# Kernel optimization log

Measured on AMD Instinct MI355X. Metric: run time of the kernel, lower is better.

The kernel has to match this reference:

```python
import jax, jax.numpy as jnp
import numpy as np

K = 3  # involution kernel size


def dwconv3x3(x, w, b):
    # x: [B,C,H,W], w: [C,1,3,3] (depthwise, groups=C), b: [C]
    y = jax.lax.conv_general_dilated(
        x, w, window_strides=(1, 1), padding='SAME',
        dimension_numbers=('NCHW', 'OIHW', 'NCHW'),
        feature_group_count=x.shape[1])
    return y + b[None, :, None, None]


def conv1x1(x, w, b):
    # x: [B,C,H,W], w: [O,C], b: [O]
    return jnp.einsum('oc,bchw->bohw', w, x) + b[None, :, None, None]


def extract_patches(x):
    # x: [B,C,H,W] -> [B,C,K*K,H,W], zero-padded 'same' 3x3 neighborhoods
    B, C, H, W = x.shape
    p = (K - 1) // 2
    xp = jnp.pad(x, ((0, 0), (0, 0), (p, p), (p, p)))
    return jnp.stack([xp[:, :, i:i + H, j:j + W]
                      for i in range(K) for j in range(K)], axis=2)


def involution(x, w_red, b_red, w_span, b_span):
    # dynamic per-pixel kernels: [B, K*K, H, W]
    kern = conv1x1(jax.nn.relu(conv1x1(x, w_red, b_red)), w_span, b_span)
    patches = extract_patches(x)                 # [B,C,KK,H,W]
    return jnp.einsum('bkhw,bckhw->bchw', kern, patches)


def setup_inputs() -> dict:
    key = jax.random.key(0)
    ks = jax.random.split(key, 10)
    dim, red = 256, 64  # reduction ratio 4
    B, H, W = 8, 64, 64
    s = 0.05
    return {
        'x': jax.random.normal(ks[0], (B, dim, H, W), jnp.float32),
        'w_in': jax.random.normal(ks[1], (dim, 1, 3, 3), jnp.float32) * s,
        'b_in': jax.random.normal(ks[2], (dim,), jnp.float32) * s,
        'w_red': jax.random.normal(ks[3], (red, dim), jnp.float32) * s,
        'b_red': jax.random.normal(ks[4], (red,), jnp.float32) * s,
        'w_span': jax.random.normal(ks[5], (K * K, red), jnp.float32) * s,
        'b_span': jax.random.normal(ks[6], (K * K,), jnp.float32) * s,
        'w_out': jax.random.normal(ks[7], (dim, 1, 3, 3), jnp.float32) * s,
        'b_out': jax.random.normal(ks[8], (dim,), jnp.float32) * s,
    }


def reference(x, w_in, b_in, w_red, b_red, w_span, b_span, w_out, b_out):
    x = dwconv3x3(x, w_in, b_in)
    x = involution(x, w_red, b_red, w_span, b_span)
    x = dwconv3x3(x, w_out, b_out)
    return x
```

## Files before the change

kernel.cpp:

```cpp
#include <hip/hip_runtime.h>

#define BB 8
#define CC 256
#define HH 64
#define WW 64
#define RED 64
#define HW 4096
#define XS 68
#define LS 68

__global__ __launch_bounds__(256) void transpose_wred(const float* __restrict__ w_red,
                                                      float* __restrict__ wt) {
    int idx = blockIdx.x * 256 + threadIdx.x;
    int o = idx >> 8, c = idx & 255;
    wt[c * RED + o] = w_red[idx];
}

__global__ __launch_bounds__(512, 4) void dw_kern(const float* __restrict__ x,
                                                  const float* __restrict__ w_in,
                                                  const float* __restrict__ b_in,
                                                  const float* __restrict__ wt,
                                                  const float* __restrict__ b_red,
                                                  const float* __restrict__ w_span,
                                                  const float* __restrict__ b_span,
                                                  float* __restrict__ kern) {
    __shared__ float smem[4352 + 2 * 4096];
    float* xs   = smem;
    float* wbuf = smem + 4352;
    float* part = smem;

    const int t  = threadIdx.x;
    const int bx = blockIdx.x;
    const int h  = ((bx & 7) << 3) | (bx >> 3);
    const int b  = blockIdx.y;
    const int px = t & 63;
    const int og = t >> 6;
    const int o0 = __builtin_amdgcn_readfirstlane(og << 3);
    const int q  = t & 15;
    const int w0 = q << 2;
    const int cr = t >> 4;

    float4 pv[2][3]; float plf[2][3], prt[2][3];
    float4 wv0, wv1;

    auto loadX = [&](int c0) {
        #pragma unroll
        for (int s = 0; s < 2; s++) {
            const int cc = c0 + s * 32 + cr;
            const float* xp = x + ((size_t)(b * CC + cc)) * HW;
            #pragma unroll
            for (int ky = 0; ky < 3; ky++) {
                int hh = h + ky - 1;
                if (hh < 0 || hh >= HH) {
                    pv[s][ky] = make_float4(0.f, 0.f, 0.f, 0.f);
                    plf[s][ky] = 0.f; prt[s][ky] = 0.f;
                    continue;
                }
                const float* row = xp + hh * WW + w0;
                pv[s][ky]  = *(const float4*)row;
                plf[s][ky] = (w0 > 0)      ? row[-1] : 0.f;
                prt[s][ky] = (w0 + 4 < WW) ? row[4]  : 0.f;
            }
        }
    };
    auto loadW = [&](int c0) {
        const float* wp = wt + c0 * RED + t * 8;
        wv0 = *(const float4*)wp;
        wv1 = *(const float4*)(wp + 4);
    };
    auto computeX = [&](int c0) {
        #pragma unroll
        for (int s = 0; s < 2; s++) {
            const int cl = s * 32 + cr;
            const int cc = c0 + cl;
            const float* wp = w_in + cc * 9;
            const float bb = b_in[cc];
            float4 a4 = make_float4(bb, bb, bb, bb);
            #pragma unroll
            for (int ky = 0; ky < 3; ky++) {
                float4 v = pv[s][ky];
                float lf = plf[s][ky], rt = prt[s][ky];
                float k0 = wp[ky * 3 + 0], k1 = wp[ky * 3 + 1], k2 = wp[ky * 3 + 2];
                a4.x = fmaf(k0, lf,  a4.x); a4.y = fmaf(k0, v.x, a4.y);
                a4.z = fmaf(k0, v.y, a4.z); a4.w = fmaf(k0, v.z, a4.w);
                a4.x = fmaf(k1, v.x, a4.x); a4.y = fmaf(k1, v.y, a4.y);
                a4.z = fmaf(k1, v.z, a4.z); a4.w = fmaf(k1, v.w, a4.w);
                a4.x = fmaf(k2, v.y, a4.x); a4.y = fmaf(k2, v.z, a4.y);
                a4.z = fmaf(k2, v.w, a4.z); a4.w = fmaf(k2, rt,  a4.w);
            }
            *(float4*)&xs[cl * XS + w0] = a4;
        }
    };
    auto storeW = [&](int buf) {
        float* wb = wbuf + buf * 4096 + t * 8;
        *(float4*)wb = wv0;
        *(float4*)(wb + 4) = wv1;
    };

    float acc[8];
    #pragma unroll
    for (int i = 0; i < 8; i++) acc[i] = 0.f;

    loadX(0); loadW(0);
    computeX(0); storeW(0);
    __syncthreads();

    for (int k = 0; k < 4; k++) {
        if (k < 3) { loadX((k + 1) << 6); loadW((k + 1) << 6); }
        const float* wb = wbuf + (k & 1) * 4096 + o0;
        #pragma unroll 8
        for (int c = 0; c < 64; c++) {
            float xv = xs[c * XS + px];
            float4 wa = *(const float4*)(wb + c * 64);
            float4 wc = *(const float4*)(wb + c * 64 + 4);
            acc[0] = fmaf(wa.x, xv, acc[0]);
            acc[1] = fmaf(wa.y, xv, acc[1]);
            acc[2] = fmaf(wa.z, xv, acc[2]);
            acc[3] = fmaf(wa.w, xv, acc[3]);
            acc[4] = fmaf(wc.x, xv, acc[4]);
            acc[5] = fmaf(wc.y, xv, acc[5]);
            acc[6] = fmaf(wc.z, xv, acc[6]);
            acc[7] = fmaf(wc.w, xv, acc[7]);
        }
        __syncthreads();
        if (k < 3) {
            computeX((k + 1) << 6);
            storeW((k + 1) & 1);
            __syncthreads();
        }
    }

    float kk[9];
    #pragma unroll
    for (int j = 0; j < 9; j++) kk[j] = 0.f;
    #pragma unroll
    for (int i = 0; i < 8; i++) {
        float r = fmaxf(acc[i] + b_red[o0 + i], 0.f);
        #pragma unroll
        for (int j = 0; j < 9; j++) kk[j] = fmaf(w_span[j * RED + o0 + i], r, kk[j]);
    }
    #pragma unroll
    for (int j = 0; j < 9; j++) part[(og * 9 + j) * 64 + px] = kk[j];
    __syncthreads();
    if (og == 0) {
        float* kp = kern + (size_t)b * 9 * HW + h * WW + px;
        #pragma unroll
        for (int j = 0; j < 9; j++) {
            float s = b_span[j];
            #pragma unroll
            for (int g = 0; g < 8; g++) s += part[(g * 9 + j) * 64 + px];
            kp[j * HW] = s;
        }
    }
}

__global__ __launch_bounds__(256) void invol_dw(const float* __restrict__ x,
                                                const float* __restrict__ w_in,
                                                const float* __restrict__ b_in,
                                                const float* __restrict__ kern,
                                                const float* __restrict__ w_out,
                                                const float* __restrict__ b_out,
                                                float* __restrict__ out) {
    __shared__ float xs[HH * LS];
    __shared__ float x1s[HH * LS];
    const int t  = threadIdx.x;
    const int q  = t & 15;
    const int w0 = q << 2;
    const int r  = t >> 4;
    const int c = blockIdx.x, b = blockIdx.y;
    const float* xp = x + ((size_t)(b * CC + c)) * HW;

    #pragma unroll
    for (int i = 0; i < 4; i++) {
        int h = r + (i << 4);
        *(float4*)&xs[h * LS + w0] = *(const float4*)(xp + h * WW + w0);
    }
    __syncthreads();

    {
        const float* wp = w_in + c * 9;
        const float bb = b_in[c];
        #pragma unroll
        for (int i = 0; i < 4; i++) {
            int h = r + (i << 4);
            float4 acc = make_float4(bb, bb, bb, bb);
            #pragma unroll
            for (int ky = 0; ky < 3; ky++) {
                int hh = h + ky - 1;
                if (hh < 0 || hh >= HH) continue;
                const float* row = &xs[hh * LS + w0];
                float4 v = *(const float4*)row;
                float lf = (w0 > 0)      ? row[-1] : 0.f;
                float rt = (w0 + 4 < WW) ? row[4]  : 0.f;
                float k0 = wp[ky * 3 + 0], k1 = wp[ky * 3 + 1], k2 = wp[ky * 3 + 2];
                acc.x = fmaf(k0, lf,  acc.x); acc.y = fmaf(k0, v.x, acc.y);
                acc.z = fmaf(k0, v.y, acc.z); acc.w = fmaf(k0, v.z, acc.w);
                acc.x = fmaf(k1, v.x, acc.x); acc.y = fmaf(k1, v.y, acc.y);
                acc.z = fmaf(k1, v.z, acc.z); acc.w = fmaf(k1, v.w, acc.w);
                acc.x = fmaf(k2, v.y, acc.x); acc.y = fmaf(k2, v.z, acc.y);
                acc.z = fmaf(k2, v.w, acc.z); acc.w = fmaf(k2, rt,  acc.w);
            }
            *(float4*)&x1s[h * LS + w0] = acc;
        }
    }
    __syncthreads();

    const float* kp = kern + (size_t)b * 9 * HW;
    #pragma unroll
    for (int i = 0; i < 4; i++) {
        int h  = r + (i << 4);
        int hw = h * WW + w0;
        float4 acc = make_float4(0.f, 0.f, 0.f, 0.f);
        #pragma unroll
        for (int ky = 0; ky < 3; ky++) {
            int hh = h + ky - 1;
            if (hh < 0 || hh >= HH) continue;
            const float* row = &x1s[hh * LS + w0];
            float4 v = *(const float4*)row;
            float lf = (w0 > 0)      ? row[-1] : 0.f;
            float rt = (w0 + 4 < WW) ? row[4]  : 0.f;
            float4 k0 = *(const float4*)(kp + (ky * 3 + 0) * HW + hw);
            float4 k1 = *(const float4*)(kp + (ky * 3 + 1) * HW + hw);
            float4 k2 = *(const float4*)(kp + (ky * 3 + 2) * HW + hw);
            acc.x = fmaf(k0.x, lf,  acc.x); acc.y = fmaf(k0.y, v.x, acc.y);
            acc.z = fmaf(k0.z, v.y, acc.z); acc.w = fmaf(k0.w, v.z, acc.w);
            acc.x = fmaf(k1.x, v.x, acc.x); acc.y = fmaf(k1.y, v.y, acc.y);
            acc.z = fmaf(k1.z, v.z, acc.z); acc.w = fmaf(k1.w, v.w, acc.w);
            acc.x = fmaf(k2.x, v.y, acc.x); acc.y = fmaf(k2.y, v.z, acc.y);
            acc.z = fmaf(k2.z, v.w, acc.z); acc.w = fmaf(k2.w, rt,  acc.w);
        }
        *(float4*)&xs[h * LS + w0] = acc;
    }
    __syncthreads();

    const float* wp = w_out + c * 9;
    const float bb = b_out[c];
    float* op = out + ((size_t)(b * CC + c)) * HW;
    #pragma unroll
    for (int i = 0; i < 4; i++) {
        int h = r + (i << 4);
        float4 acc = make_float4(bb, bb, bb, bb);
        #pragma unroll
        for (int ky = 0; ky < 3; ky++) {
            int hh = h + ky - 1;
            if (hh < 0 || hh >= HH) continue;
            const float* row = &xs[hh * LS + w0];
            float4 v = *(const float4*)row;
            float lf = (w0 > 0)      ? row[-1] : 0.f;
            float rt = (w0 + 4 < WW) ? row[4]  : 0.f;
            float k0 = wp[ky * 3 + 0], k1 = wp[ky * 3 + 1], k2 = wp[ky * 3 + 2];
            acc.x = fmaf(k0, lf,  acc.x); acc.y = fmaf(k0, v.x, acc.y);
            acc.z = fmaf(k0, v.y, acc.z); acc.w = fmaf(k0, v.z, acc.w);
            acc.x = fmaf(k1, v.x, acc.x); acc.y = fmaf(k1, v.y, acc.y);
            acc.z = fmaf(k1, v.z, acc.z); acc.w = fmaf(k1, v.w, acc.w);
            acc.x = fmaf(k2, v.y, acc.x); acc.y = fmaf(k2, v.z, acc.y);
            acc.z = fmaf(k2, v.w, acc.z); acc.w = fmaf(k2, rt,  acc.w);
        }
        *(float4*)(op + h * WW + w0) = acc;
    }
}

extern "C" void kernel_launch(void* const* d_in, const int* in_sizes, int n_in,
                              void* d_out, int out_size, void* d_ws, size_t ws_size,
                              hipStream_t stream) {
    const float* x      = (const float*)d_in[0];
    const float* w_in   = (const float*)d_in[1];
    const float* b_in   = (const float*)d_in[2];
    const float* w_red  = (const float*)d_in[3];
    const float* b_red  = (const float*)d_in[4];
    const float* w_span = (const float*)d_in[5];
    const float* b_span = (const float*)d_in[6];
    const float* w_out  = (const float*)d_in[7];
    const float* b_out  = (const float*)d_in[8];
    float* out = (float*)d_out;

    float* ws   = (float*)d_ws;
    float* kern = ws;
    float* wt   = kern + (size_t)BB * 9 * HW;

    transpose_wred<<<64, 256, 0, stream>>>(w_red, wt);
    dw_kern<<<dim3(HH, BB), 512, 0, stream>>>(x, w_in, b_in, wt, b_red,
                                              w_span, b_span, kern);
    invol_dw<<<dim3(CC, BB), 256, 0, stream>>>(x, w_in, b_in, kern,
                                               w_out, b_out, out);
}
```

Before: 155.8 us.

## Compute channel-reduction 1x1 conv with bf16 MFMA instead of scalar FMAs

The 256->64 reduction conv in dw_kern now runs on matrix cores via mfma_f32_16x16x32_bf16. The dwconv output is stored to LDS as bf16 in a transposed layout, and the reduction weights are pre-swizzled into a bf16 MFMA B-fragment layout by a setup kernel, so B fragments are loaded straight from global memory into registers. This removes the scalar FMA inner loop and the LDS weight double-buffering. In exchange it adds bf16 rounding error to the reduction result and scatters 2-byte LDS stores in the transposed write.

```diff
diff --git a/kernel.cpp b/kernel.cpp
--- a/kernel.cpp
+++ b/kernel.cpp
@@ -6,42 +6,53 @@
 #define WW 64
 #define RED 64
 #define HW 4096
-#define XS 68
+#define AST 72
 #define LS 68
 
-__global__ __launch_bounds__(256) void transpose_wred(const float* __restrict__ w_red,
-                                                      float* __restrict__ wt) {
-    int idx = blockIdx.x * 256 + threadIdx.x;
-    int o = idx >> 8, c = idx & 255;
-    wt[c * RED + o] = w_red[idx];
+typedef __attribute__((ext_vector_type(8))) short s8v;
+typedef __attribute__((ext_vector_type(4))) float f4v;
+
+__device__ __forceinline__ unsigned short f2bf(float f) {
+    unsigned u = __float_as_uint(f);
+    u += 0x7fff + ((u >> 16) & 1);
+    return (unsigned short)(u >> 16);
+}
+
+__global__ __launch_bounds__(256) void build_wtf(const float* __restrict__ w_red,
+                                                 unsigned short* __restrict__ wtf) {
+    int e = blockIdx.x * 256 + threadIdx.x;
+    int j = e & 7, l = (e >> 3) & 63, nt = (e >> 9) & 3, kbg = e >> 11;
+    int o = nt * 16 + (l & 15);
+    int c = kbg * 32 + ((l >> 4) & 3) * 8 + j;
+    wtf[e] = f2bf(w_red[o * CC + c]);
 }
 
 __global__ __launch_bounds__(512, 4) void dw_kern(const float* __restrict__ x,
                                                   const float* __restrict__ w_in,
                                                   const float* __restrict__ b_in,
-                                                  const float* __restrict__ wt,
+                                                  const unsigned short* __restrict__ wtf,
                                                   const float* __restrict__ b_red,
                                                   const float* __restrict__ w_span,
                                                   const float* __restrict__ b_span,
                                                   float* __restrict__ kern) {
-    __shared__ float smem[4352 + 2 * 4096];
-    float* xs   = smem;
-    float* wbuf = smem + 4352;
-    float* part = smem;
+    alignas(16) __shared__ char smem[16640 + 18432];
+    unsigned short* xs = (unsigned short*)smem;
+    float* r_lds = (float*)smem;
+    float* part  = (float*)(smem + 16640);
 
     const int t  = threadIdx.x;
     const int bx = blockIdx.x;
     const int h  = ((bx & 7) << 3) | (bx >> 3);
     const int b  = blockIdx.y;
-    const int px = t & 63;
-    const int og = t >> 6;
-    const int o0 = __builtin_amdgcn_readfirstlane(og << 3);
+    const int l  = t & 63;
+    const int wv = t >> 6;
+    const int mt = wv & 3, nh = wv >> 2;
+    const int m0 = mt << 4;
     const int q  = t & 15;
     const int w0 = q << 2;
     const int cr = t >> 4;
 
     float4 pv[2][3]; float plf[2][3], prt[2][3];
-    float4 wv0, wv1;
 
     auto loadX = [&](int c0) {
         #pragma unroll
@@ -63,12 +74,7 @@
             }
         }
     };
-    auto loadW = [&](int c0) {
-        const float* wp = wt + c0 * RED + t * 8;
-        wv0 = *(const float4*)wp;
-        wv1 = *(const float4*)(wp + 4);
-    };
-    auto computeX = [&](int c0) {
+    auto computeA = [&](int c0) {
         #pragma unroll
         for (int s = 0; s < 2; s++) {
             const int cl = s * 32 + cr;
@@ -88,61 +94,71 @@
                 a4.x = fmaf(k2, v.y, a4.x); a4.y = fmaf(k2, v.z, a4.y);
                 a4.z = fmaf(k2, v.w, a4.z); a4.w = fmaf(k2, rt,  a4.w);
             }
-            *(float4*)&xs[cl * XS + w0] = a4;
+            xs[(w0 + 0) * AST + cl] = f2bf(a4.x);
+            xs[(w0 + 1) * AST + cl] = f2bf(a4.y);
+            xs[(w0 + 2) * AST + cl] = f2bf(a4.z);
+            xs[(w0 + 3) * AST + cl] = f2bf(a4.w);
         }
     };
-    auto storeW = [&](int buf) {
-        float* wb = wbuf + buf * 4096 + t * 8;
-        *(float4*)wb = wv0;
-        *(float4*)(wb + 4) = wv1;
+
+    s8v bfr[2][2];
+    auto loadB = [&](int k) {
+        #pragma unroll
+        for (int kb = 0; kb < 2; kb++)
+            #pragma unroll
+            for (int ntl = 0; ntl < 2; ntl++) {
+                int nt = (nh << 1) + ntl;
+                int kbg = (k << 1) + kb;
+                bfr[kb][ntl] = *(const s8v*)(wtf + (((kbg * 4 + nt) * 64 + l) << 3));
+            }
     };
 
-    float acc[8];
-    #pragma unroll
-    for (int i = 0; i < 8; i++) acc[i] = 0.f;
-
-    loadX(0); loadW(0);
-    computeX(0); storeW(0);
-    __syncthreads();
-
+    f4v acc[2] = {{0.f, 0.f, 0.f, 0.f}, {0.f, 0.f, 0.f, 0.f}};
+
+    loadX(0); loadB(0);
     for (int k = 0; k < 4; k++) {
-        if (k < 3) { loadX((k + 1) << 6); loadW((k + 1) << 6); }
-        const float* wb = wbuf + (k & 1) * 4096 + o0;
-        #pragma unroll 8
-        for (int c = 0; c < 64; c++) {
-            float xv = xs[c * XS + px];
-            float4 wa = *(const float4*)(wb + c * 64);
-            float4 wc = *(const float4*)(wb + c * 64 + 4);
-            acc[0] = fmaf(wa.x, xv, acc[0]);
-            acc[1] = fmaf(wa.y, xv, acc[1]);
-            acc[2] = fmaf(wa.z, xv, acc[2]);
-            acc[3] = fmaf(wa.w, xv, acc[3]);
-            acc[4] = fmaf(wc.x, xv, acc[4]);
-            acc[5] = fmaf(wc.y, xv, acc[5]);
-            acc[6] = fmaf(wc.z, xv, acc[6]);
-            acc[7] = fmaf(wc.w, xv, acc[7]);
-        }
+        computeA(k << 6);
+        if (k < 3) loadX((k + 1) << 6);
         __syncthreads();
-        if (k < 3) {
-            computeX((k + 1) << 6);
-            storeW((k + 1) & 1);
-            __syncthreads();
-        }
-    }
-
+        #pragma unroll
+        for (int kb = 0; kb < 2; kb++) {
+            const unsigned short* ap =
+                xs + (m0 + (l & 15)) * AST + (kb << 5) + ((l >> 4) & 3) * 8;
+            s8v av = *(const s8v*)ap;
+            #pragma unroll
+            for (int ntl = 0; ntl < 2; ntl++)
+                acc[ntl] = __builtin_amdgcn_mfma_f32_16x16x32_bf16(
+                    av, bfr[kb][ntl], acc[ntl], 0, 0, 0);
+        }
+        if (k < 3) loadB(k + 1);
+        __syncthreads();
+    }
+
+    #pragma unroll
+    for (int ntl = 0; ntl < 2; ntl++) {
+        int o = ((nh << 1) + ntl) * 16 + (l & 15);
+        int pxr = m0 + ((l >> 4) & 3) * 4;
+        #pragma unroll
+        for (int i = 0; i < 4; i++)
+            r_lds[o * 65 + pxr + i] = acc[ntl][i];
+    }
+    __syncthreads();
+
+    const int px = t & 63;
+    const int o0 = __builtin_amdgcn_readfirstlane(wv << 3);
     float kk[9];
     #pragma unroll
     for (int j = 0; j < 9; j++) kk[j] = 0.f;
     #pragma unroll
     for (int i = 0; i < 8; i++) {
-        float r = fmaxf(acc[i] + b_red[o0 + i], 0.f);
+        float r = fmaxf(r_lds[(o0 + i) * 65 + px] + b_red[o0 + i], 0.f);
         #pragma unroll
         for (int j = 0; j < 9; j++) kk[j] = fmaf(w_span[j * RED + o0 + i], r, kk[j]);
     }
     #pragma unroll
-    for (int j = 0; j < 9; j++) part[(og * 9 + j) * 64 + px] = kk[j];
-    __syncthreads();
-    if (og == 0) {
+    for (int j = 0; j < 9; j++) part[(wv * 9 + j) * 64 + px] = kk[j];
+    __syncthreads();
+    if (wv == 0) {
         float* kp = kern + (size_t)b * 9 * HW + h * WW + px;
         #pragma unroll
         for (int j = 0; j < 9; j++) {
@@ -276,10 +292,10 @@
 
     float* ws   = (float*)d_ws;
     float* kern = ws;
-    float* wt   = kern + (size_t)BB * 9 * HW;
-
-    transpose_wred<<<64, 256, 0, stream>>>(w_red, wt);
-    dw_kern<<<dim3(HH, BB), 512, 0, stream>>>(x, w_in, b_in, wt, b_red,
+    unsigned short* wtf = (unsigned short*)(kern + (size_t)BB * 9 * HW);
+
+    build_wtf<<<64, 256, 0, stream>>>(w_red, wtf);
+    dw_kern<<<dim3(HH, BB), 512, 0, stream>>>(x, w_in, b_in, wtf, b_red,
                                               w_span, b_span, kern);
     invol_dw<<<dim3(CC, BB), 256, 0, stream>>>(x, w_in, b_in, kern,
                                                w_out, b_out, out);
```

Result: faster. 136.4 us (-12.4%).
